# Kernel optimization log

Hardware: AMD Instinct MI355X
Metric: run time of the kernel (lower is better)

The kernel has to match this reference:

```python
import jax, jax.numpy as jnp
import numpy as np

N, E, R = 50000, 800000, 8
EMB, PROJ, H, OUT = 512, 256, 256, 200


def rgcn_conv(x, src, dst, rel, W, root, bias):
    # PyG RGCNConv: per-relation linear transform, mean aggregation per relation
    # over incoming edges, summed across relations, plus root transform + bias.
    n = x.shape[0]
    r, _, out_dim = W.shape
    h = jnp.einsum('ni,rio->nro', x, W)            # [N,R,out] per-relation transforms
    msgs = h[src, rel]                             # [E,out] gather per-edge messages
    seg = dst * r + rel                            # combined (node, relation) segment id
    sums = jax.ops.segment_sum(msgs, seg, num_segments=n * r)
    cnt = jax.ops.segment_sum(jnp.ones((src.shape[0],), x.dtype), seg, num_segments=n * r)
    mean = sums / jnp.maximum(cnt, 1.0)[:, None]
    agg = mean.reshape(n, r, out_dim).sum(axis=1)  # sum over relations
    return agg + x @ root + bias


def setup_inputs() -> dict:
    key = jax.random.key(0)
    ks = jax.random.split(key, 16)
    inp = {
        'embeddings': jax.random.normal(ks[0], (N, EMB), jnp.float32),
        'node_indices': jnp.arange(N, dtype=jnp.int64) if jax.config.jax_enable_x64 else jnp.arange(N, dtype=jnp.int32),
        'src': jax.random.randint(ks[1], (E,), 0, N),
        'dst': jax.random.randint(ks[2], (E,), 0, N),
        'rel': jax.random.randint(ks[3], (E,), 0, R),
        'neg_src': jax.random.randint(ks[4], (E,), 0, N),
        'neg_dst': jax.random.randint(ks[5], (E,), 0, N),
        'neg_rel': jax.random.randint(ks[6], (E,), 0, R),
        # learned parameters
        'Wp': jax.random.normal(ks[7], (EMB, PROJ), jnp.float32) * 0.04,
        'bp': jnp.zeros((PROJ,), jnp.float32),
        'W0': jax.random.normal(ks[8], (R, PROJ, H), jnp.float32) * 0.06,
        'root0': jax.random.normal(ks[9], (PROJ, H), jnp.float32) * 0.06,
        'b0': jnp.zeros((H,), jnp.float32),
        'W1': jax.random.normal(ks[10], (R, H, H), jnp.float32) * 0.06,
        'root1': jax.random.normal(ks[11], (H, H), jnp.float32) * 0.06,
        'b1': jnp.zeros((H,), jnp.float32),
        'W2': jax.random.normal(ks[12], (R, H, OUT), jnp.float32) * 0.06,
        'root2': jax.random.normal(ks[13], (H, OUT), jnp.float32) * 0.06,
        'b2': jnp.zeros((OUT,), jnp.float32),
        'rel_emb': jax.random.normal(ks[14], (R, OUT), jnp.float32),
    }
    return inp


def reference(embeddings, node_indices, src, dst, rel, neg_src, neg_dst, neg_rel,
              Wp, bp, W0, root0, b0, W1, root1, b1, W2, root2, b2, rel_emb):
    # projection: Linear per modality, then reorder rows by node index (sort)
    proj = embeddings @ Wp + bp                        # [N,PROJ]
    x = jnp.zeros_like(proj).at[node_indices].set(proj)
    # stacked RGCN encoder with relu between layers (no relu on last)
    x = jax.nn.relu(rgcn_conv(x, src, dst, rel, W0, root0, b0))
    x = jax.nn.relu(rgcn_conv(x, src, dst, rel, W1, root1, b1))
    out = rgcn_conv(x, src, dst, rel, W2, root2, b2)   # [N,OUT]
    # DistMult decoder over positive + negative triples
    s = jnp.concatenate([src, neg_src])
    o = jnp.concatenate([dst, neg_dst])
    r = jnp.concatenate([rel, neg_rel])
    scores = jnp.sum(out[s] * rel_emb[r] * out[o], axis=-1)  # [2E]
    return out, scores
```

## Files before the change

### kernel.cpp

```cpp
#include <hip/hip_runtime.h>
#include <stdint.h>

#define NN 50000
#define NE 800000
#define NR 8
#define EMBD 512
#define PROJD 256
#define HIDD 256
#define OUTD 200
#define NSEG (NN * NR)
#define CSR_CAP 1536

typedef _Float16 half8 __attribute__((ext_vector_type(8)));
typedef _Float16 half4 __attribute__((ext_vector_type(4)));
typedef float f32x4 __attribute__((ext_vector_type(4)));

__device__ __forceinline__ void gload16(const void* g, void* l) {
    __builtin_amdgcn_global_load_lds(
        reinterpret_cast<const __attribute__((address_space(1))) uint32_t*>(
            reinterpret_cast<uintptr_t>(g)),
        reinterpret_cast<__attribute__((address_space(3))) uint32_t*>(
            reinterpret_cast<uintptr_t>(l)),
        16, 0, 0);
}


__global__ void count_edges(const int* __restrict__ dst, const int* __restrict__ rel,
                            int* __restrict__ cnt, int E) {
    int e = blockIdx.x * 256 + threadIdx.x;
    if (e >= E) return;
    atomicAdd(&cnt[dst[e] * NR + rel[e]], 1);
}

__global__ __launch_bounds__(512) void scan1(const int* __restrict__ cnt, int* __restrict__ offs,
                                             int* __restrict__ bsums, int n) {
    __shared__ int sm[512];
    int tid = threadIdx.x;
    int g = blockIdx.x * 512 + tid;
    int v = (g < n) ? cnt[g] : 0;
    sm[tid] = v;
    __syncthreads();
    for (int o = 1; o < 512; o <<= 1) {
        int t = (tid >= o) ? sm[tid - o] : 0;
        __syncthreads();
        sm[tid] += t;
        __syncthreads();
    }
    if (g < n) offs[g] = sm[tid] - v;
    if (tid == 511) bsums[blockIdx.x] = sm[511];
}

__global__ __launch_bounds__(1024) void scan2(const int* __restrict__ bsums, int* __restrict__ bpref, int nb) {
    __shared__ int sm[1024];
    int tid = threadIdx.x;
    int v = (tid < nb) ? bsums[tid] : 0;
    sm[tid] = v;
    __syncthreads();
    for (int o = 1; o < 1024; o <<= 1) {
        int t = (tid >= o) ? sm[tid - o] : 0;
        __syncthreads();
        sm[tid] += t;
        __syncthreads();
    }
    if (tid < nb) bpref[tid] = sm[tid] - v;
}

__global__ __launch_bounds__(512) void scan3(int* __restrict__ offs, int* __restrict__ cursor,
                                             const int* __restrict__ bpref, int n, int total) {
    int g = blockIdx.x * 512 + threadIdx.x;
    if (g < n) {
        int v = offs[g] + bpref[blockIdx.x];
        offs[g] = v;
        cursor[g] = v;
    } else if (g <= n + 1024) {
        offs[g] = total;
    }
}

__global__ void scatter_edges(const int* __restrict__ dst, const int* __restrict__ rel,
                              const int* __restrict__ src, int* __restrict__ cursor,
                              int* __restrict__ csr, int E) {
    int e = blockIdx.x * 256 + threadIdx.x;
    if (e >= E) return;
    int seg = dst[e] * NR + rel[e];
    int pos = atomicAdd(&cursor[seg], 1);
    csr[pos] = src[e];
}


__global__ void f32_to_f16_vec(const float* __restrict__ in, _Float16* __restrict__ out, long n4) {
    long i = (long)blockIdx.x * 256 + threadIdx.x;
    long stride = (long)gridDim.x * 256;
    for (; i < n4; i += stride) {
        float4 v = ((const float4*)in)[i];
        half4 h;
        h[0] = (_Float16)v.x; h[1] = (_Float16)v.y; h[2] = (_Float16)v.z; h[3] = (_Float16)v.w;
        ((half4*)out)[i] = h;
    }
}

__global__ __launch_bounds__(256) void build_bt(const float* __restrict__ S0, int K0,
                                                const float* __restrict__ S1,
                                                _Float16* __restrict__ Bt, int N, int K) {
    __shared__ float tile[32][33];
    const int kb = blockIdx.x * 32, nb = blockIdx.y * 32;
    const int tx = threadIdx.x & 31, ty = threadIdx.x >> 5;
#pragma unroll
    for (int i = 0; i < 32; i += 8) {
        int k = kb + ty + i, n = nb + tx;
        float v = 0.f;
        if (k < K && n < N) v = (k < K0) ? S0[(size_t)k * N + n] : S1[(size_t)(k - K0) * N + n];
        tile[ty + i][tx] = v;
    }
    __syncthreads();
#pragma unroll
    for (int i = 0; i < 32; i += 8) {
        int n = nb + ty + i, k = kb + tx;
        if (n < N && k < K) Bt[(size_t)n * K + k] = (_Float16)tile[tx][ty + i];
    }
}


template <bool RELU, bool LAST>
__global__ __launch_bounds__(512, 4) void rgcn_layer(
    const _Float16* __restrict__ x, const _Float16* __restrict__ Bt,
    const int* __restrict__ csr, const int* __restrict__ offs,
    const float* __restrict__ bias,
    _Float16* __restrict__ C16, int ldc, float* __restrict__ C32, int N) {
    __shared__ _Float16 As[64 * 256];
    __shared__ _Float16 Bs[2][256 * 32];
    __shared__ int offs_lds[520];
    __shared__ int csr_lds[CSR_CAP];
    const int tid = threadIdx.x;
    const int lane = tid & 63, wave = tid >> 6;
    const int lane32 = tid & 31, hw = tid >> 5;
    const int half_base = lane & 32;
    const int l15 = lane & 15, q = lane >> 4;
    const int m0 = blockIdx.x * 64;
    const int segbase = m0 * NR;

    for (int i = tid; i < 513; i += 512) offs_lds[i] = offs[segbase + i];
    __syncthreads();
    const int e0 = offs_lds[0];
    const int e1 = offs_lds[512];
    const int ecnt = min(e1 - e0, CSR_CAP);
    for (int i = tid; i < ecnt; i += 512) csr_lds[i] = csr[e0 + i];
    __syncthreads();

    auto stage = [&](int buf, int g) {
        int kbase = g * 32;
#pragma unroll
        for (int h = 0; h < 2; ++h) {
            int s = lane + h * 64;
            int n = wave * 32 + (s >> 2);
            int c4 = s & 3;
            int nn = n < N ? n : N - 1;
            gload16(Bt + (size_t)nn * 2304 + kbase + ((c4 ^ (n & 3)) << 3),
                    &Bs[buf][wave * 1024 + h * 512]);
        }
    };

    f32x4 acc[4][2] = {};
    stage(0, 0);
    int cur = 0;
    for (int seg = 0; seg < 9; ++seg) {
#pragma unroll
        for (int u = 0; u < 4; ++u) {
            int lr = u * 16 + hw;
            int nd = m0 + lr;
            if (nd >= NN) nd = NN - 1;
            half8 hv;
            if (seg == 0) {
                hv = *(const half8*)(x + (size_t)nd * 256 + lane32 * 8);
            } else {
                int sb = lr * NR + seg - 1;
                int o0 = offs_lds[sb], o1 = offs_lds[sb + 1];
                int n = o1 - o0;
                if (n < 0) n = 0;
                if (n == 0) {
#pragma unroll
                    for (int z = 0; z < 8; ++z) hv[z] = (_Float16)0.f;
                } else {
                    bool staged = (o1 - e0) <= CSR_CAP;
                    int fi = o0 + (lane32 < n ? lane32 : n - 1);
                    int idxv = staged ? csr_lds[fi - e0] : csr[fi];
                    half8 sA = {}, sB = {};
                    int nb = n < 32 ? n : 32;
                    int e = 0;
                    for (; e + 4 <= nb; e += 4) {
                        int s0 = __shfl(idxv, half_base + e);
                        int s1 = __shfl(idxv, half_base + e + 1);
                        int s2 = __shfl(idxv, half_base + e + 2);
                        int s3 = __shfl(idxv, half_base + e + 3);
                        half8 v0 = *(const half8*)(x + (size_t)s0 * 256 + lane32 * 8);
                        half8 v1 = *(const half8*)(x + (size_t)s1 * 256 + lane32 * 8);
                        half8 v2 = *(const half8*)(x + (size_t)s2 * 256 + lane32 * 8);
                        half8 v3 = *(const half8*)(x + (size_t)s3 * 256 + lane32 * 8);
                        sA += v0 + v1;
                        sB += v2 + v3;
                    }
                    for (; e < nb; ++e) {
                        int s0 = __shfl(idxv, half_base + e);
                        half8 v0 = *(const half8*)(x + (size_t)s0 * 256 + lane32 * 8);
                        sA += v0;
                    }
                    for (int e2 = 32; e2 < n; ++e2) {
                        int s2i = staged ? csr_lds[o0 - e0 + e2] : csr[o0 + e2];
                        half8 v = *(const half8*)(x + (size_t)s2i * 256 + lane32 * 8);
                        sB += v;
                    }
                    _Float16 hinv = (_Float16)(1.0f / (float)n);
                    hv = (sA + sB) * hinv;
                }
            }
            *(half8*)((char*)As + lr * 512 + ((lane32 ^ (lr & 31)) << 4)) = hv;
        }
        asm volatile("s_waitcnt lgkmcnt(0)" ::: "memory");
        __builtin_amdgcn_s_barrier();
        asm volatile("" ::: "memory");
#pragma unroll
        for (int ch = 0; ch < 8; ++ch) {
            int g = seg * 8 + ch;
            if (g < 71) {
                stage(cur ^ 1, g + 1);
                asm volatile("s_waitcnt vmcnt(2)" ::: "memory");
            } else {
                asm volatile("s_waitcnt vmcnt(0)" ::: "memory");
            }
            half8 a[4], b[2];
#pragma unroll
            for (int i = 0; i < 4; ++i) {
                int row = i * 16 + l15;
                int ck = ch * 4 + q;
                a[i] = *(const half8*)((const char*)As + row * 512 + ((ck ^ (row & 31)) << 4));
            }
#pragma unroll
            for (int j = 0; j < 2; ++j) {
                int n = wave * 32 + j * 16 + l15;
                b[j] = *(const half8*)((const char*)&Bs[cur][0] + n * 64 + ((q ^ (n & 3)) << 4));
            }
            __builtin_amdgcn_s_setprio(1);
#pragma unroll
            for (int i = 0; i < 4; ++i)
#pragma unroll
                for (int j = 0; j < 2; ++j)
                    acc[i][j] = __builtin_amdgcn_mfma_f32_16x16x32_f16(a[i], b[j], acc[i][j], 0, 0, 0);
            __builtin_amdgcn_s_setprio(0);
            cur ^= 1;
        }
        asm volatile("s_waitcnt lgkmcnt(0)" ::: "memory");
        __builtin_amdgcn_s_barrier();
        asm volatile("" ::: "memory");
    }
#pragma unroll
    for (int j = 0; j < 2; ++j) {
        int cc = wave * 32 + j * 16 + l15;
        if (cc >= N) continue;
        float bv = bias[cc];
#pragma unroll
        for (int i = 0; i < 4; ++i) {
            int rbase = m0 + i * 16 + q * 4;
#pragma unroll
            for (int t = 0; t < 4; ++t) {
                int rr = rbase + t;
                if (rr >= NN) continue;
                float v = acc[i][j][t] + bv;
                if (RELU) v = fmaxf(v, 0.f);
                C16[(size_t)rr * ldc + cc] = (_Float16)v;
                if (LAST) C32[(size_t)rr * ldc + cc] = v;
            }
        }
    }
}


template <bool BIAS, bool ACC_IN, bool FINAL, bool RELU, bool LAST, bool SCATTER>
__global__ __launch_bounds__(256) void gemm16(
    const _Float16* __restrict__ A, int lda,
    const _Float16* __restrict__ Bt, int ldb,
    const float* __restrict__ bias, const int* __restrict__ sidx,
    _Float16* __restrict__ Cacc,
    _Float16* __restrict__ C16, int ldc, float* __restrict__ C32,
    int M, int N, int K) {
    __shared__ _Float16 As[2][4096];
    __shared__ _Float16 Bs[2][4096];
    const int tid = threadIdx.x;
    const int lane = tid & 63, wave = tid >> 6;
    const int wm = wave >> 1, wn = wave & 1;
    const int q = lane >> 4, l15 = lane & 15;
    const int m0 = blockIdx.y * 128, n0 = blockIdx.x * 128;
    const int wbase = wave * 512;
    f32x4 acc[4][4] = {};

    auto stage = [&](int buf, int k0) {
#pragma unroll
        for (int h = 0; h < 2; ++h) {
            int s = tid + h * 256;
            int r = s >> 2, c = s & 3;
            int cs = c ^ ((r >> 2) & 3);
            int ga = m0 + r; if (ga >= M) ga = M - 1;
            gload16(A + (size_t)ga * lda + k0 + cs * 8, &As[buf][wbase + h * 2048]);
            int gb = n0 + r; if (gb >= N) gb = N - 1;
            gload16(Bt + (size_t)gb * ldb + k0 + cs * 8, &Bs[buf][wbase + h * 2048]);
        }
    };

    const int nk = K >> 5;
    stage(0, 0);
    int cur = 0;
    for (int kt = 0; kt < nk; ++kt) {
        if (kt + 1 < nk) {
            stage(cur ^ 1, (kt + 1) << 5);
            asm volatile("s_waitcnt vmcnt(4)" ::: "memory");
        } else {
            asm volatile("s_waitcnt vmcnt(0)" ::: "memory");
        }
        __builtin_amdgcn_s_barrier();
        asm volatile("" ::: "memory");
        half8 a[4], b[4];
#pragma unroll
        for (int i = 0; i < 4; ++i) {
            int row = wm * 64 + i * 16 + l15;
            a[i] = *(const half8*)&As[cur][row * 32 + ((q ^ ((row >> 2) & 3)) << 3)];
            int col = wn * 64 + i * 16 + l15;
            b[i] = *(const half8*)&Bs[cur][col * 32 + ((q ^ ((col >> 2) & 3)) << 3)];
        }
#pragma unroll
        for (int i = 0; i < 4; ++i)
#pragma unroll
            for (int j = 0; j < 4; ++j)
                acc[i][j] = __builtin_amdgcn_mfma_f32_16x16x32_f16(a[i], b[j], acc[i][j], 0, 0, 0);
        asm volatile("s_waitcnt lgkmcnt(0)" ::: "memory");
        __builtin_amdgcn_s_barrier();
        asm volatile("" ::: "memory");
        cur ^= 1;
    }
#pragma unroll
    for (int i = 0; i < 4; ++i) {
        int rbase = m0 + wm * 64 + i * 16 + q * 4;
#pragma unroll
        for (int j = 0; j < 4; ++j) {
            int cc = n0 + wn * 64 + j * 16 + l15;
            if (cc >= N) continue;
#pragma unroll
            for (int t = 0; t < 4; ++t) {
                int rr = rbase + t;
                if (rr >= M) continue;
                float v = acc[i][j][t];
                if (BIAS) v += bias[cc];
                if (ACC_IN) v += (float)Cacc[(size_t)rr * 256 + cc];
                if (!FINAL) {
                    Cacc[(size_t)rr * 256 + cc] = (_Float16)v;
                } else {
                    if (RELU) v = fmaxf(v, 0.f);
                    int ro = SCATTER ? sidx[rr] : rr;
                    C16[(size_t)ro * ldc + cc] = (_Float16)v;
                    if (LAST) C32[(size_t)ro * ldc + cc] = v;
                }
            }
        }
    }
}


__global__ __launch_bounds__(256) void decoder16(
    const _Float16* __restrict__ out16, const _Float16* __restrict__ rel16,
    const int* __restrict__ src, const int* __restrict__ dst, const int* __restrict__ rel,
    const int* __restrict__ nsrc, const int* __restrict__ ndst, const int* __restrict__ nrel,
    float* __restrict__ scores) {
    __shared__ _Float16 rel_lds[NR * OUTD];
    if (threadIdx.x < 200) {
        int rr = threadIdx.x / 25, cc = threadIdx.x % 25;
        *(half8*)&rel_lds[rr * OUTD + cc * 8] = *(const half8*)(rel16 + (size_t)rr * OUTD + cc * 8);
    }
    __syncthreads();
    int gid = blockIdx.x * 256 + threadIdx.x;
    int t = gid >> 3, lq = gid & 7;
    if (t >= 2 * NE) return;
    int s, o, r;
    if (t < NE) { s = src[t]; o = dst[t]; r = rel[t]; }
    else { int u = t - NE; s = nsrc[u]; o = ndst[u]; r = nrel[u]; }
    const half8* ps = (const half8*)(out16 + (size_t)s * OUTD);
    const half8* po = (const half8*)(out16 + (size_t)o * OUTD);
    const _Float16* pr = rel_lds + r * OUTD;
    half8 hacc0 = {}, hacc1 = {};
#pragma unroll
    for (int it = 0; it < 4; ++it) {
        int c = it * 8 + lq;
        if (c < 25) {
            half8 a = ps[c], d = po[c];
            half8 b = *(const half8*)(pr + c * 8);
            half8 p = a * b * d;
            if (it & 1) hacc1 += p; else hacc0 += p;
        }
    }
    float acc = 0.f;
#pragma unroll
    for (int u = 0; u < 8; ++u) acc += (float)hacc0[u] + (float)hacc1[u];
#pragma unroll
    for (int off = 4; off; off >>= 1) acc += __shfl_xor(acc, off);
    if (lq == 0) scores[t] = acc;
}


extern "C" void kernel_launch(void* const* d_in, const int* in_sizes, int n_in,
                              void* d_out, int out_size, void* d_ws, size_t ws_size,
                              hipStream_t stream) {
    const float* emb   = (const float*)d_in[0];
    const int*   nidx  = (const int*)d_in[1];
    const int*   src   = (const int*)d_in[2];
    const int*   dst   = (const int*)d_in[3];
    const int*   rel   = (const int*)d_in[4];
    const int*   nsrc  = (const int*)d_in[5];
    const int*   ndst  = (const int*)d_in[6];
    const int*   nrel  = (const int*)d_in[7];
    const float* Wp    = (const float*)d_in[8];
    const float* bp    = (const float*)d_in[9];
    const float* W0    = (const float*)d_in[10];
    const float* root0 = (const float*)d_in[11];
    const float* b0    = (const float*)d_in[12];
    const float* W1    = (const float*)d_in[13];
    const float* root1 = (const float*)d_in[14];
    const float* b1    = (const float*)d_in[15];
    const float* W2    = (const float*)d_in[16];
    const float* root2 = (const float*)d_in[17];
    const float* b2    = (const float*)d_in[18];
    const float* rele  = (const float*)d_in[19];
    (void)in_sizes; (void)n_in; (void)out_size; (void)ws_size;

    float* out    = (float*)d_out;
    float* scores = out + (size_t)NN * OUTD;

    auto align = [](size_t x) { return (x + 255) & ~(size_t)255; };
    char* p = (char*)d_ws;
    auto alloc = [&](size_t bytes) -> char* {
        char* q = p; p += align(bytes); return q;
    };
    _Float16* emb16  = (_Float16*)alloc((size_t)NN * EMBD * 2);
    _Float16* xbufA  = (_Float16*)alloc((size_t)NN * 256 * 2);
    _Float16* xbufB  = (_Float16*)alloc((size_t)NN * 256 * 2);
    _Float16* out16  = xbufB;
    _Float16* Bt0 = (_Float16*)alloc((size_t)256 * 2304 * 2);
    _Float16* Bt1 = (_Float16*)alloc((size_t)256 * 2304 * 2);
    _Float16* Bt2 = (_Float16*)alloc((size_t)256 * 2304 * 2);
    _Float16* BtP = (_Float16*)alloc((size_t)256 * EMBD * 2);
    _Float16* rel16 = (_Float16*)alloc((size_t)NR * OUTD * 2);
    int*   cnt    = (int*)alloc((size_t)NSEG * 4);
    int*   cursor = (int*)alloc((size_t)NSEG * 4);
    int*   offs   = (int*)alloc((size_t)(NSEG + 1032) * 4);
    int*   csr    = (int*)alloc((size_t)NE * 4);
    int*   bsums  = (int*)alloc(4096);
    int*   bpref  = (int*)alloc(4096);

    hipMemsetAsync(cnt, 0, (size_t)NSEG * 4, stream);
    count_edges<<<(NE + 255) / 256, 256, 0, stream>>>(dst, rel, cnt, NE);
    const int NB = (NSEG + 511) / 512;
    scan1<<<NB, 512, 0, stream>>>(cnt, offs, bsums, NSEG);
    scan2<<<1, 1024, 0, stream>>>(bsums, bpref, NB);
    scan3<<<NB + 3, 512, 0, stream>>>(offs, cursor, bpref, NSEG, NE);
    scatter_edges<<<(NE + 255) / 256, 256, 0, stream>>>(dst, rel, src, cursor, csr, NE);

    f32_to_f16_vec<<<2048, 256, 0, stream>>>(emb, emb16, (long)NN * EMBD / 4);
    f32_to_f16_vec<<<2, 256, 0, stream>>>(rele, rel16, (long)NR * OUTD / 4);
    build_bt<<<dim3(16, 8), 256, 0, stream>>>(Wp, EMBD, nullptr, BtP, PROJD, EMBD);
    build_bt<<<dim3(72, 8), 256, 0, stream>>>(root0, 256, W0, Bt0, HIDD, 2304);
    build_bt<<<dim3(72, 8), 256, 0, stream>>>(root1, 256, W1, Bt1, HIDD, 2304);
    build_bt<<<dim3(72, 7), 256, 0, stream>>>(root2, 256, W2, Bt2, OUTD, 2304);

    {
        dim3 g(2, (NN + 127) / 128);
        gemm16<true, false, true, false, false, true><<<g, 256, 0, stream>>>(
            emb16, EMBD, BtP, EMBD, bp, nidx, nullptr, xbufA, 256, nullptr, NN, 256, EMBD);
    }

    const int GL = (NN + 63) / 64;
    rgcn_layer<true, false><<<GL, 512, 0, stream>>>(xbufA, Bt0, csr, offs, b0,
                                                    xbufB, 256, nullptr, HIDD);
    rgcn_layer<true, false><<<GL, 512, 0, stream>>>(xbufB, Bt1, csr, offs, b1,
                                                    xbufA, 256, nullptr, HIDD);
    rgcn_layer<false, true><<<GL, 512, 0, stream>>>(xbufA, Bt2, csr, offs, b2,
                                                    out16, OUTD, out, OUTD);

    decoder16<<<(2 * NE * 8 + 255) / 256, 256, 0, stream>>>(out16, rel16, src, dst, rel,
                                                            nsrc, ndst, nrel, scores);
}
```

Baseline: 826.6 us.

## Bucket decoder triples by source node block for gather locality

Adds a counting-sort pass (histogram, scan, scatter) that groups the 1.6M decoder triples by src>>6 buckets, so the decoder reads them in an order where the source rows of out16 are clustered. The goal is better L2 reuse on the source-side gathers. The cost is three extra kernels with atomics, writes of four permuted index arrays, and scattered score writes through st[].

```diff
diff --git a/kernel.cpp b/kernel.cpp
--- a/kernel.cpp
+++ b/kernel.cpp
@@ -10,6 +10,7 @@
 #define OUTD 200
 #define NSEG (NN * NR)
 #define CSR_CAP 1536
+#define NBK 784
 
 typedef _Float16 half8 __attribute__((ext_vector_type(8)));
 typedef _Float16 half4 __attribute__((ext_vector_type(4)));
@@ -85,6 +86,45 @@
     int seg = dst[e] * NR + rel[e];
     int pos = atomicAdd(&cursor[seg], 1);
     csr[pos] = src[e];
+}
+
+
+__global__ void hist_triples(const int* __restrict__ src, const int* __restrict__ nsrc,
+                             int* __restrict__ hist) {
+    int t = blockIdx.x * 256 + threadIdx.x;
+    if (t >= 2 * NE) return;
+    int s = (t < NE) ? src[t] : nsrc[t - NE];
+    atomicAdd(&hist[s >> 6], 1);
+}
+
+__global__ __launch_bounds__(1024) void scan_hist(const int* __restrict__ hist,
+                                                  int* __restrict__ cur) {
+    __shared__ int sm[1024];
+    int tid = threadIdx.x;
+    int v = (tid < NBK) ? hist[tid] : 0;
+    sm[tid] = v;
+    __syncthreads();
+    for (int o = 1; o < 1024; o <<= 1) {
+        int t = (tid >= o) ? sm[tid - o] : 0;
+        __syncthreads();
+        sm[tid] += t;
+        __syncthreads();
+    }
+    if (tid < NBK) cur[tid] = sm[tid] - v;
+}
+
+__global__ void scatter_triples(const int* __restrict__ src, const int* __restrict__ dst,
+                                const int* __restrict__ rel, const int* __restrict__ nsrc,
+                                const int* __restrict__ ndst, const int* __restrict__ nrel,
+                                int* __restrict__ cur, int* __restrict__ ss, int* __restrict__ so,
+                                int* __restrict__ sr, int* __restrict__ st) {
+    int t = blockIdx.x * 256 + threadIdx.x;
+    if (t >= 2 * NE) return;
+    int s, o, r;
+    if (t < NE) { s = src[t]; o = dst[t]; r = rel[t]; }
+    else { int u = t - NE; s = nsrc[u]; o = ndst[u]; r = nrel[u]; }
+    int pos = atomicAdd(&cur[s >> 6], 1);
+    ss[pos] = s; so[pos] = o; sr[pos] = r; st[pos] = t;
 }
 
 
@@ -363,11 +403,10 @@
 }
 
 
-__global__ __launch_bounds__(256) void decoder16(
+__global__ __launch_bounds__(256) void decoder16s(
     const _Float16* __restrict__ out16, const _Float16* __restrict__ rel16,
-    const int* __restrict__ src, const int* __restrict__ dst, const int* __restrict__ rel,
-    const int* __restrict__ nsrc, const int* __restrict__ ndst, const int* __restrict__ nrel,
-    float* __restrict__ scores) {
+    const int* __restrict__ ss, const int* __restrict__ so, const int* __restrict__ sr,
+    const int* __restrict__ st, float* __restrict__ scores) {
     __shared__ _Float16 rel_lds[NR * OUTD];
     if (threadIdx.x < 200) {
         int rr = threadIdx.x / 25, cc = threadIdx.x % 25;
@@ -377,9 +416,7 @@
     int gid = blockIdx.x * 256 + threadIdx.x;
     int t = gid >> 3, lq = gid & 7;
     if (t >= 2 * NE) return;
-    int s, o, r;
-    if (t < NE) { s = src[t]; o = dst[t]; r = rel[t]; }
-    else { int u = t - NE; s = nsrc[u]; o = ndst[u]; r = nrel[u]; }
+    int s = ss[t], o = so[t], r = sr[t];
     const half8* ps = (const half8*)(out16 + (size_t)s * OUTD);
     const half8* po = (const half8*)(out16 + (size_t)o * OUTD);
     const _Float16* pr = rel_lds + r * OUTD;
@@ -399,7 +436,7 @@
     for (int u = 0; u < 8; ++u) acc += (float)hacc0[u] + (float)hacc1[u];
 #pragma unroll
     for (int off = 4; off; off >>= 1) acc += __shfl_xor(acc, off);
-    if (lq == 0) scores[t] = acc;
+    if (lq == 0) scores[st[t]] = acc;
 }
 
 
@@ -451,6 +488,12 @@
     int*   csr    = (int*)alloc((size_t)NE * 4);
     int*   bsums  = (int*)alloc(4096);
     int*   bpref  = (int*)alloc(4096);
+    int*   ss     = (int*)alloc((size_t)2 * NE * 4);
+    int*   so     = (int*)alloc((size_t)2 * NE * 4);
+    int*   sr     = (int*)alloc((size_t)2 * NE * 4);
+    int*   st     = (int*)alloc((size_t)2 * NE * 4);
+    int*   bhist  = (int*)alloc(NBK * 4);
+    int*   bcur   = (int*)alloc(NBK * 4);
 
     hipMemsetAsync(cnt, 0, (size_t)NSEG * 4, stream);
     count_edges<<<(NE + 255) / 256, 256, 0, stream>>>(dst, rel, cnt, NE);
@@ -460,6 +503,12 @@
     scan3<<<NB + 3, 512, 0, stream>>>(offs, cursor, bpref, NSEG, NE);
     scatter_edges<<<(NE + 255) / 256, 256, 0, stream>>>(dst, rel, src, cursor, csr, NE);
 
+    hipMemsetAsync(bhist, 0, NBK * 4, stream);
+    hist_triples<<<(2 * NE + 255) / 256, 256, 0, stream>>>(src, nsrc, bhist);
+    scan_hist<<<1, 1024, 0, stream>>>(bhist, bcur);
+    scatter_triples<<<(2 * NE + 255) / 256, 256, 0, stream>>>(src, dst, rel, nsrc, ndst, nrel,
+                                                              bcur, ss, so, sr, st);
+
     f32_to_f16_vec<<<2048, 256, 0, stream>>>(emb, emb16, (long)NN * EMBD / 4);
     f32_to_f16_vec<<<2, 256, 0, stream>>>(rele, rel16, (long)NR * OUTD / 4);
     build_bt<<<dim3(16, 8), 256, 0, stream>>>(Wp, EMBD, nullptr, BtP, PROJD, EMBD);
@@ -481,6 +530,6 @@
     rgcn_layer<false, true><<<GL, 512, 0, stream>>>(xbufA, Bt2, csr, offs, b2,
                                                     out16, OUTD, out, OUTD);
 
-    decoder16<<<(2 * NE * 8 + 255) / 256, 256, 0, stream>>>(out16, rel16, src, dst, rel,
-                                                            nsrc, ndst, nrel, scores);
-}
+    decoder16s<<<(2 * NE * 8 + 255) / 256, 256, 0, stream>>>(out16, rel16, ss, so, sr, st,
+                                                             scores);
+}
```

Result: slower. 1.542 ms (+86.6%).
